# Kernel optimization log

Hardware: AMD Instinct MI355X
Metric: run time of the kernel (lower is better)

The kernel has to match this reference:

```python
import jax, jax.numpy as jnp
from jax import lax
import numpy as np

B, M = 16384, 200            # flattened batch (B*TT), tokens per observation
NUM_LAYERS, GW, GH = 22, 11, 11
CNN_CH, HIDDEN = 128, 512
ACTION_NVEC = (9, 10)

MAX_VEC = jnp.array([9.0, 1.0, 1.0, 10.0, 3.0, 254.0, 1.0, 1.0, 235.0, 8.0, 9.0,
                     250.0, 29.0, 1.0, 1.0, 8.0, 1.0, 1.0, 6.0, 3.0, 1.0, 2.0],
                    jnp.float32)[None, :, None, None]  # [1,22,1,1]


def setup_inputs() -> dict:
    key = jax.random.key(0)
    ks = jax.random.split(key, 16)
    # compose coords byte so x,y nibbles are valid grid indices (0..10)
    xs = jax.random.randint(ks[0], (B, M), 0, GW)
    ys = jax.random.randint(ks[1], (B, M), 0, GH)
    coords = xs * 16 + ys
    atr = jax.random.randint(ks[2], (B, M), 0, NUM_LAYERS)
    val = jax.random.randint(ks[3], (B, M), 0, 11)
    observations = jnp.stack([coords, atr, val], axis=-1).astype(jnp.int32)  # [B,M,3]

    def nrm(k, shape, std=0.02):
        return (jax.random.normal(k, shape, jnp.float32) * std)

    return {
        "observations": observations,
        "conv1_w": nrm(ks[4], (CNN_CH, NUM_LAYERS, 5, 5)),
        "conv1_b": jnp.zeros((CNN_CH,), jnp.float32),
        "conv2_w": nrm(ks[5], (CNN_CH, CNN_CH, 3, 3)),
        "conv2_b": jnp.zeros((CNN_CH,), jnp.float32),
        "fc_w": nrm(ks[6], (HIDDEN // 2, CNN_CH)),
        "fc_b": jnp.zeros((HIDDEN // 2,), jnp.float32),
        "self_w": nrm(ks[7], (HIDDEN // 2, NUM_LAYERS)),
        "self_b": jnp.zeros((HIDDEN // 2,), jnp.float32),
        "actor0_w": nrm(ks[8], (ACTION_NVEC[0], HIDDEN), std=0.01),
        "actor0_b": jnp.zeros((ACTION_NVEC[0],), jnp.float32),
        "actor1_w": nrm(ks[9], (ACTION_NVEC[1], HIDDEN), std=0.01),
        "actor1_b": jnp.zeros((ACTION_NVEC[1],), jnp.float32),
        "value_w": nrm(ks[10], (1, HIDDEN)),
        "value_b": jnp.zeros((1,), jnp.float32),
    }


def reference(observations, conv1_w, conv1_b, conv2_w, conv2_b, fc_w, fc_b,
              self_w, self_b, actor0_w, actor0_b, actor1_w, actor1_b,
              value_w, value_b):
    obs = jnp.where(observations == 255, 0, observations)
    coords = obs[..., 0]
    xs = (coords >> 4) & 15
    ys = coords & 15
    atr = obs[..., 1]
    vals = obs[..., 2].astype(jnp.float32)           # [B,M]
    Bt = obs.shape[0]
    b_idx = jnp.broadcast_to(jnp.arange(Bt)[:, None], vals.shape)
    # masked scatter into dense grid (all tokens valid after 255->0 clamp)
    box = jnp.zeros((Bt, NUM_LAYERS, GW, GH), jnp.float32)
    box = box.at[b_idx, atr, xs, ys].set(vals, mode="drop")
    feats = box / MAX_VEC                            # [B,22,11,11]

    self_f = jax.nn.relu(feats[:, :, 5, 5] @ self_w.T + self_b)  # [B,256]

    dn = ("NCHW", "OIHW", "NCHW")
    h = lax.conv_general_dilated(feats, conv1_w, (3, 3), "VALID", dimension_numbers=dn)
    h = jax.nn.relu(h + conv1_b[None, :, None, None])            # [B,128,3,3]
    h = lax.conv_general_dilated(h, conv2_w, (1, 1), "VALID", dimension_numbers=dn)
    h = jax.nn.relu(h + conv2_b[None, :, None, None])            # [B,128,1,1]
    h = h.reshape(Bt, -1)
    cnn_f = jax.nn.relu(h @ fc_w.T + fc_b)                       # [B,256]

    hidden = jnp.concatenate([self_f, cnn_f], axis=1)            # [B,512]
    logits0 = hidden @ actor0_w.T + actor0_b
    logits1 = hidden @ actor1_w.T + actor1_b
    value = hidden @ value_w.T + value_b
    return (logits0, logits1, value)
```

## Files before the change

### kernel.cpp

```cpp
#include <hip/hip_runtime.h>

typedef unsigned short u16;
typedef __attribute__((ext_vector_type(8))) short short8;
typedef __attribute__((ext_vector_type(4))) float f32x4;

#define MFMA16(a, b, c) __builtin_amdgcn_mfma_f32_16x16x32_bf16((a), (b), (c), 0, 0, 0)

__device__ __forceinline__ u16 f2bf(float f) {
    unsigned u = __float_as_uint(f);
    unsigned r = (u + 0x7FFFu + ((u >> 16) & 1u)) >> 16;
    return (u16)r;
}

__device__ const float MAXV[22] = {9.f, 1.f, 1.f, 10.f, 3.f, 254.f, 1.f, 1.f, 235.f, 8.f, 9.f,
                                   250.f, 29.f, 1.f, 1.f, 8.f, 1.f, 1.f, 6.f, 3.f, 1.f, 2.f};

__global__ void prep_kernel(
    const float* c1w, const float* c1b, const float* c2w, const float* c2b,
    const float* fcw, const float* fcb, const float* sfw, const float* sfb,
    const float* a0w, const float* a0b, const float* a1w, const float* a1b,
    const float* vw, const float* vb,
    u16* W1F, u16* W2F, u16* FCF, u16* SELFF, u16* HEADF, float* BIAS)
{
    int idx = blockIdx.x * 256 + threadIdx.x;
    if (idx < 73728) {
        int grp = idx >> 9, off = idx & 511;
        int g = grp / 18, ks = grp - g * 18;
        int l = off >> 3, e = off & 7;
        int n = g * 16 + (l & 15);
        int k = ks * 32 + ((l >> 4) << 3) + e;
        float v = 0.f;
        if (k < 550) { int c = k / 25; v = c1w[n * 550 + k] * (1.0f / MAXV[c]); }
        W1F[idx] = f2bf(v);
    } else if (idx < 221184) {
        int j = idx - 73728;
        int grp = j >> 9, off = j & 511;
        int g = grp / 36, ks = grp - g * 36;
        int l = off >> 3, e = off & 7;
        int oc = g * 16 + (l & 15);
        int k = ks * 32 + ((l >> 4) << 3) + e;
        W2F[j] = f2bf(c2w[oc * 1152 + (k & 127) * 9 + (k >> 7)]);
    } else if (idx < 253952) {
        int j = idx - 221184;
        int grp = j >> 9, off = j & 511;
        int g = grp >> 2, kc = grp & 3;
        int l = off >> 3, e = off & 7;
        int n = g * 16 + (l & 15);
        int k = kc * 32 + ((l >> 4) << 3) + e;
        FCF[j] = f2bf(fcw[n * 128 + k]);
    } else if (idx < 262144) {
        int j = idx - 253952;
        int g = j >> 9, off = j & 511;
        int l = off >> 3, e = off & 7;
        int n = g * 16 + (l & 15);
        int k = ((l >> 4) << 3) + e;
        float v = (k < 22) ? sfw[n * 22 + k] * (1.0f / MAXV[k]) : 0.f;
        SELFF[j] = f2bf(v);
    } else if (idx < 278528) {
        int j = idx - 262144;
        int grp = j >> 9, off = j & 511;
        int g = grp >> 4, ks = grp & 15;
        int l = off >> 3, e = off & 7;
        int n = g * 16 + (l & 15);
        int k = ks * 32 + ((l >> 4) << 3) + e;
        float v = 0.f;
        if (n < 9) v = a0w[n * 512 + k];
        else if (n < 19) v = a1w[(n - 9) * 512 + k];
        else if (n == 19) v = vw[k];
        HEADF[j] = f2bf(v);
    } else if (idx < 279328) {
        int j = idx - 278528;
        float v = 0.f;
        if (j < 128) v = c1b[j];
        else if (j < 256) v = c2b[j - 128];
        else if (j < 512) v = fcb[j - 256];
        else if (j < 768) v = sfb[j - 512];
        else {
            int j2 = j - 768;
            if (j2 < 9) v = a0b[j2]; else if (j2 < 19) v = a1b[j2 - 9]; else if (j2 == 19) v = vb[0];
        }
        BIAS[j] = v;
    }
}

__global__ __launch_bounds__(256, 4) void k12_kernel(
    const int* __restrict__ obs, const u16* __restrict__ W1F,
    const float* __restrict__ BIAS, u16* __restrict__ h1F, u16* __restrict__ s22g)
{
    __shared__ __align__(16) u16 A[19968];
    const int tid = threadIdx.x, w = tid >> 6, l = tid & 63;
    const int s0 = blockIdx.x * 4;

    const int* myobs = obs + (long)(s0 + w) * 600;
    int tk[4][3];
    #pragma unroll
    for (int r = 0; r < 4; ++r) {
        int m = r * 64 + l; int mm = m < 200 ? m : 0;
        tk[r][0] = myobs[mm * 3]; tk[r][1] = myobs[mm * 3 + 1]; tk[r][2] = myobs[mm * 3 + 2];
    }

    {
        short8 z = {0, 0, 0, 0, 0, 0, 0, 0};
        int base = w * 621;
        int cnt = (w == 3) ? 633 : 621;
        for (int i = l; i < cnt; i += 64) *(short8*)(A + (base + i) * 8) = z;
    }
    __builtin_amdgcn_sched_barrier(0);

    #pragma unroll
    for (int r = 0; r < 4; ++r) {
        int m = r * 64 + l;
        int c = tk[r][0], a = tk[r][1], v = tk[r][2];
        c = (c == 255) ? 0 : c; a = (a == 255) ? 0 : a; v = (v == 255) ? 0 : v;
        int xs = (c >> 4) & 15, ys = c & 15;
        int ok = (m < 200) & ((unsigned)a < 22u) & (xs < 11) & (ys < 11);
        if (ok) {
            u16 bv = f2bf((float)v);
            int bcol = a * 25;
            #pragma unroll
            for (int ox = 0; ox < 3; ++ox) {
                int kx = xs - 3 * ox;
                if ((unsigned)kx > 4u) continue;
                #pragma unroll
                for (int oy = 0; oy < 3; ++oy) {
                    int ky = ys - 3 * oy;
                    if ((unsigned)ky > 4u) continue;
                    int row = w * 9 + ox * 3 + oy;
                    A[row * 552 + bcol + kx * 5 + ky] = bv;
                }
            }
        }
        __builtin_amdgcn_sched_barrier(0);
    }
    if (l < 32) {
        int row = w * 9 + 4;
        s22g[(s0 + w) * 32 + l] = A[row * 552 + l * 25 + 12];
    }
    __syncthreads();

    int Aoff[3];
    #pragma unroll
    for (int mt = 0; mt < 3; ++mt) {
        int row = mt * 16 + (l & 15);
        row = row < 36 ? row : 35;
        Aoff[mt] = (row * 552 + ((l >> 4) << 3)) << 1;
    }
    const u16* Wp0 = W1F + ((w * 2 + 0) * 18 << 9) + l * 8;
    const u16* Wp1 = W1F + ((w * 2 + 1) * 18 << 9) + l * 8;

    f32x4 acc[3][2];
    const f32x4 fz = {0.f, 0.f, 0.f, 0.f};
    #pragma unroll
    for (int i = 0; i < 3; ++i) { acc[i][0] = fz; acc[i][1] = fz; }

    short8 cb0 = *(const short8*)(Wp0);
    short8 cb1 = *(const short8*)(Wp1);
    short8 nb0 = *(const short8*)(Wp0 + 512);
    short8 nb1 = *(const short8*)(Wp1 + 512);
    __builtin_amdgcn_s_setprio(1);
    #pragma unroll
    for (int ks = 0; ks < 18; ++ks) {
        short8 t0 = cb0, t1 = cb1;
        if (ks < 16) {
            t0 = *(const short8*)(Wp0 + (ks + 2) * 512);
            t1 = *(const short8*)(Wp1 + (ks + 2) * 512);
        }
        short8 a0 = *(const short8*)((const char*)A + Aoff[0] + ks * 64);
        short8 a1 = *(const short8*)((const char*)A + Aoff[1] + ks * 64);
        short8 a2 = *(const short8*)((const char*)A + Aoff[2] + ks * 64);
        acc[0][0] = MFMA16(a0, cb0, acc[0][0]);
        acc[0][1] = MFMA16(a0, cb1, acc[0][1]);
        acc[1][0] = MFMA16(a1, cb0, acc[1][0]);
        acc[1][1] = MFMA16(a1, cb1, acc[1][1]);
        acc[2][0] = MFMA16(a2, cb0, acc[2][0]);
        acc[2][1] = MFMA16(a2, cb1, acc[2][1]);
        cb0 = nb0; cb1 = nb1; nb0 = t0; nb1 = t1;
    }
    __builtin_amdgcn_s_setprio(0);

    #pragma unroll
    for (int mt = 0; mt < 3; ++mt) {
        #pragma unroll
        for (int nt = 0; nt < 2; ++nt) {
            int col = w * 32 + nt * 16 + (l & 15);
            float bias = BIAS[col];
            #pragma unroll
            for (int r = 0; r < 4; ++r) {
                int row = mt * 16 + ((l >> 4) << 2) + r;
                if (row < 36) {
                    int ds = row / 9;
                    int pos = row - ds * 9;
                    int s = s0 + ds;
                    float v = acc[mt][nt][r] + bias;
                    v = v > 0.f ? v : 0.f;
                    long ad = (long)(s >> 4) * 18432 + (pos * 4 + w) * 512 +
                              (s & 15) * 8 + (((col >> 3) & 3) << 7) + (col & 7);
                    h1F[ad] = f2bf(v);
                }
            }
        }
    }
}

__global__ __launch_bounds__(256, 2) void k3a_kernel(
    const u16* __restrict__ h1F, const u16* __restrict__ W2F,
    const float* __restrict__ BIAS, u16* __restrict__ a3F)
{
    const int tid = threadIdx.x, w = tid >> 6, l = tid & 63;
    const int sb = blockIdx.x * 2, s0 = blockIdx.x * 32;
    const float* c2b = BIAS + 128;
    const f32x4 fz = {0.f, 0.f, 0.f, 0.f};
    f32x4 acc[2][2];
    acc[0][0] = fz; acc[0][1] = fz; acc[1][0] = fz; acc[1][1] = fz;

    const u16* A0p = h1F + (long)(sb + 0) * 18432 + l * 8;
    const u16* A1p = h1F + (long)(sb + 1) * 18432 + l * 8;
    const u16* B0p = W2F + ((w * 2 + 0) * 36 << 9) + l * 8;
    const u16* B1p = W2F + ((w * 2 + 1) * 36 << 9) + l * 8;

    short8 ra0[3], ra1[3], rb0[3], rb1[3];
    #pragma unroll
    for (int d = 0; d < 3; ++d) {
        ra0[d] = *(const short8*)(A0p + d * 512);
        ra1[d] = *(const short8*)(A1p + d * 512);
        rb0[d] = *(const short8*)(B0p + d * 512);
        rb1[d] = *(const short8*)(B1p + d * 512);
    }
    __builtin_amdgcn_s_setprio(1);
    #pragma unroll
    for (int ks = 0; ks < 36; ++ks) {
        const int sl = ks % 3;
        short8 a0 = ra0[sl], a1 = ra1[sl], b0 = rb0[sl], b1 = rb1[sl];
        if (ks < 33) {
            ra0[sl] = *(const short8*)(A0p + (ks + 3) * 512);
            ra1[sl] = *(const short8*)(A1p + (ks + 3) * 512);
            rb0[sl] = *(const short8*)(B0p + (ks + 3) * 512);
            rb1[sl] = *(const short8*)(B1p + (ks + 3) * 512);
        }
        acc[0][0] = MFMA16(a0, b0, acc[0][0]);
        acc[0][1] = MFMA16(a0, b1, acc[0][1]);
        acc[1][0] = MFMA16(a1, b0, acc[1][0]);
        acc[1][1] = MFMA16(a1, b1, acc[1][1]);
    }
    __builtin_amdgcn_s_setprio(0);

    #pragma unroll
    for (int mt = 0; mt < 2; ++mt) {
        #pragma unroll
        for (int nt = 0; nt < 2; ++nt) {
            int col = w * 32 + nt * 16 + (l & 15);
            float bias = c2b[col];
            #pragma unroll
            for (int r = 0; r < 4; ++r) {
                int row = mt * 16 + ((l >> 4) << 2) + r;
                int s = s0 + row;
                float v = acc[mt][nt][r] + bias; v = v > 0.f ? v : 0.f;
                long ad = (long)(s >> 4) * 2048 + (col >> 5) * 512 +
                          (s & 15) * 8 + (((col >> 3) & 3) << 7) + (col & 7);
                a3F[ad] = f2bf(v);
            }
        }
    }
}

__global__ __launch_bounds__(256, 4) void k3b_kernel(
    const u16* __restrict__ a3F, const u16* __restrict__ s22g,
    const u16* __restrict__ FCF, const u16* __restrict__ SELFF,
    const u16* __restrict__ HEADF, const float* __restrict__ BIAS,
    float* __restrict__ out, int B)
{
    __shared__ __align__(16) u16 HID[16 * 520];
    const int tid = threadIdx.x, w = tid >> 6, l = tid & 63;
    const int s0 = blockIdx.x * 16;
    const float* fcb = BIAS + 256;
    const float* sfb = BIAS + 512;
    const float* hdb = BIAS + 768;
    const f32x4 fz = {0.f, 0.f, 0.f, 0.f};

    f32x4 acc8[4];
    #pragma unroll
    for (int j = 0; j < 4; ++j) acc8[j] = fz;
    #pragma unroll
    for (int kc = 0; kc < 4; ++kc) {
        short8 a = *(const short8*)(a3F + (long)blockIdx.x * 2048 + kc * 512 + l * 8);
        #pragma unroll
        for (int nt = 0; nt < 4; ++nt) {
            short8 bf = *(const short8*)(FCF + (((w * 4 + nt) * 4 + kc) << 9) + l * 8);
            acc8[nt] = MFMA16(a, bf, acc8[nt]);
        }
    }
    #pragma unroll
    for (int nt = 0; nt < 4; ++nt) {
        int col = w * 64 + nt * 16 + (l & 15);
        float bias = fcb[col];
        #pragma unroll
        for (int r = 0; r < 4; ++r) {
            int row = ((l >> 4) << 2) + r;
            float v = acc8[nt][r] + bias; v = v > 0.f ? v : 0.f;
            HID[row * 520 + 256 + col] = f2bf(v);
        }
    }

    {
        f32x4 acc9[4];
        #pragma unroll
        for (int j = 0; j < 4; ++j) acc9[j] = fz;
        short8 a = *(const short8*)(s22g + (s0 + (l & 15)) * 32 + ((l >> 4) << 3));
        #pragma unroll
        for (int nt = 0; nt < 4; ++nt) {
            short8 bs = *(const short8*)(SELFF + ((w * 4 + nt) << 9) + l * 8);
            acc9[nt] = MFMA16(a, bs, acc9[nt]);
        }
        #pragma unroll
        for (int nt = 0; nt < 4; ++nt) {
            int col = w * 64 + nt * 16 + (l & 15);
            float bias = sfb[col];
            #pragma unroll
            for (int r = 0; r < 4; ++r) {
                int row = ((l >> 4) << 2) + r;
                float v = acc9[nt][r] + bias; v = v > 0.f ? v : 0.f;
                HID[row * 520 + col] = f2bf(v);
            }
        }
    }
    __syncthreads();

    if (w < 2) {
        f32x4 hacc = fz;
        #pragma unroll
        for (int ks = 0; ks < 16; ++ks) {
            short8 a = *(const short8*)(HID + (l & 15) * 520 + ks * 32 + ((l >> 4) << 3));
            short8 b = *(const short8*)(HEADF + ((w * 16 + ks) << 9) + l * 8);
            hacc = MFMA16(a, b, hacc);
        }
        #pragma unroll
        for (int r = 0; r < 4; ++r) {
            int srow = s0 + ((l >> 4) << 2) + r;
            int col = w * 16 + (l & 15);
            float v = hacc[r] + hdb[col];
            if (col < 9) out[(long)srow * 9 + col] = v;
            else if (col < 19) out[(long)B * 9 + (long)srow * 10 + (col - 9)] = v;
            else if (col == 19) out[(long)B * 19 + srow] = v;
        }
    }
}

extern "C" void kernel_launch(void* const* d_in, const int* in_sizes, int n_in,
                              void* d_out, int out_size, void* d_ws, size_t ws_size,
                              hipStream_t stream)
{
    const int*   obs = (const int*)d_in[0];
    const float* c1w = (const float*)d_in[1];
    const float* c1b = (const float*)d_in[2];
    const float* c2w = (const float*)d_in[3];
    const float* c2b = (const float*)d_in[4];
    const float* fcw = (const float*)d_in[5];
    const float* fcb = (const float*)d_in[6];
    const float* sfw = (const float*)d_in[7];
    const float* sfb = (const float*)d_in[8];
    const float* a0w = (const float*)d_in[9];
    const float* a0b = (const float*)d_in[10];
    const float* a1w = (const float*)d_in[11];
    const float* a1b = (const float*)d_in[12];
    const float* vw  = (const float*)d_in[13];
    const float* vb  = (const float*)d_in[14];
    const int B = in_sizes[0] / 600;

    char* ws = (char*)d_ws;
    u16*   W1F   = (u16*)(ws + 0);
    u16*   W2F   = (u16*)(ws + 147456);
    u16*   FCF   = (u16*)(ws + 442368);
    u16*   SELFF = (u16*)(ws + 507904);
    u16*   HEADF = (u16*)(ws + 524288);
    float* BIAS  = (float*)(ws + 557056);
    u16*   s22g  = (u16*)(ws + 560256);
    u16*   h1F   = (u16*)(ws + 560256 + (size_t)B * 64);
    u16*   a3F   = (u16*)(ws + 560256 + (size_t)B * 64 + (size_t)B * 2304);

    prep_kernel<<<1092, 256, 0, stream>>>(c1w, c1b, c2w, c2b, fcw, fcb, sfw, sfb,
                                          a0w, a0b, a1w, a1b, vw, vb,
                                          W1F, W2F, FCF, SELFF, HEADF, BIAS);
    k12_kernel<<<B / 4, 256, 0, stream>>>(obs, W1F, BIAS, h1F, s22g);
    k3a_kernel<<<B / 32, 256, 0, stream>>>(h1F, W2F, BIAS, a3F);
    k3b_kernel<<<B / 16, 256, 0, stream>>>(a3F, s22g, FCF, SELFF, HEADF, BIAS,
                                           (float*)d_out, B);
}
```

Baseline: 71.51 us.

## Stage conv1 outputs in LDS for coalesced 16-byte stores, triple-buffer weight loads

The conv1 epilogue now writes bf16 results into the shared A buffer in the fragment layout, then has all threads copy them out as 16-byte vectors. This replaces scattered 2-byte global stores to h1F. The weight prefetch also becomes a three-deep register ring instead of two-deep, to hide more load latency behind the MFMAs. The cost is two extra barriers and reuse of LDS after the main loop.

```diff
diff --git a/kernel.cpp b/kernel.cpp
--- a/kernel.cpp
+++ b/kernel.cpp
@@ -153,50 +153,67 @@
     #pragma unroll
     for (int i = 0; i < 3; ++i) { acc[i][0] = fz; acc[i][1] = fz; }
 
-    short8 cb0 = *(const short8*)(Wp0);
-    short8 cb1 = *(const short8*)(Wp1);
-    short8 nb0 = *(const short8*)(Wp0 + 512);
-    short8 nb1 = *(const short8*)(Wp1 + 512);
+    short8 rb0[3], rb1[3];
+    #pragma unroll
+    for (int d = 0; d < 3; ++d) {
+        rb0[d] = *(const short8*)(Wp0 + d * 512);
+        rb1[d] = *(const short8*)(Wp1 + d * 512);
+    }
     __builtin_amdgcn_s_setprio(1);
     #pragma unroll
     for (int ks = 0; ks < 18; ++ks) {
-        short8 t0 = cb0, t1 = cb1;
-        if (ks < 16) {
-            t0 = *(const short8*)(Wp0 + (ks + 2) * 512);
-            t1 = *(const short8*)(Wp1 + (ks + 2) * 512);
+        const int sl = ks % 3;
+        short8 b0 = rb0[sl], b1 = rb1[sl];
+        if (ks < 15) {
+            rb0[sl] = *(const short8*)(Wp0 + (ks + 3) * 512);
+            rb1[sl] = *(const short8*)(Wp1 + (ks + 3) * 512);
         }
         short8 a0 = *(const short8*)((const char*)A + Aoff[0] + ks * 64);
         short8 a1 = *(const short8*)((const char*)A + Aoff[1] + ks * 64);
         short8 a2 = *(const short8*)((const char*)A + Aoff[2] + ks * 64);
-        acc[0][0] = MFMA16(a0, cb0, acc[0][0]);
-        acc[0][1] = MFMA16(a0, cb1, acc[0][1]);
-        acc[1][0] = MFMA16(a1, cb0, acc[1][0]);
-        acc[1][1] = MFMA16(a1, cb1, acc[1][1]);
-        acc[2][0] = MFMA16(a2, cb0, acc[2][0]);
-        acc[2][1] = MFMA16(a2, cb1, acc[2][1]);
-        cb0 = nb0; cb1 = nb1; nb0 = t0; nb1 = t1;
+        acc[0][0] = MFMA16(a0, b0, acc[0][0]);
+        acc[0][1] = MFMA16(a0, b1, acc[0][1]);
+        acc[1][0] = MFMA16(a1, b0, acc[1][0]);
+        acc[1][1] = MFMA16(a1, b1, acc[1][1]);
+        acc[2][0] = MFMA16(a2, b0, acc[2][0]);
+        acc[2][1] = MFMA16(a2, b1, acc[2][1]);
     }
     __builtin_amdgcn_s_setprio(0);
-
+    __syncthreads();
+
+    u16* R = (u16*)A;
     #pragma unroll
     for (int mt = 0; mt < 3; ++mt) {
         #pragma unroll
         for (int nt = 0; nt < 2; ++nt) {
             int col = w * 32 + nt * 16 + (l & 15);
             float bias = BIAS[col];
+            int hif = nt * 2 + ((l & 15) >> 3);
+            int ef = l & 7;
             #pragma unroll
             for (int r = 0; r < 4; ++r) {
                 int row = mt * 16 + ((l >> 4) << 2) + r;
                 if (row < 36) {
                     int ds = row / 9;
                     int pos = row - ds * 9;
-                    int s = s0 + ds;
+                    int ks = pos * 4 + w;
                     float v = acc[mt][nt][r] + bias;
                     v = v > 0.f ? v : 0.f;
-                    long ad = (long)(s >> 4) * 18432 + (pos * 4 + w) * 512 +
-                              (s & 15) * 8 + (((col >> 3) & 3) << 7) + (col & 7);
-                    h1F[ad] = f2bf(v);
+                    R[(ks * 16 + hif * 4 + ds) * 8 + ef] = f2bf(v);
                 }
+            }
+        }
+    }
+    __syncthreads();
+    {
+        const long Cbase = (long)(s0 >> 4) * 18432 + (s0 & 15) * 8;
+        #pragma unroll
+        for (int q = 0; q < 3; ++q) {
+            int slot = tid + q * 256;
+            if (slot < 576) {
+                int ks = slot >> 4, lf = slot & 15;
+                *(short8*)(h1F + Cbase + ks * 512 + (lf >> 2) * 128 + (lf & 3) * 8) =
+                    *(const short8*)(R + slot * 8);
             }
         }
     }
```

Result: faster. 68.77 us (-3.8%).
